# Performance work log

Measured on AMD Instinct MI355X. Metric: run time of the kernel, lower is better.

## Reference

```python
import jax, jax.numpy as jnp
import numpy as np

DIM = 1024
HEADS = 16
HEAD_DIM = DIM // HEADS
SCALE = HEAD_DIM ** -0.5


def setup_inputs() -> dict:
    key = jax.random.key(0)
    ks = jax.random.split(key, 9)
    B, S, D = 2, 2048, DIM
    std = 1.0 / np.sqrt(D)
    Z = jax.random.normal(ks[0], (B, S, D), dtype=jnp.float32)
    Wq = jax.random.uniform(ks[1], (D, D), jnp.float32, -std, std)
    bq = jax.random.uniform(ks[2], (D,), jnp.float32, -std, std)
    Wk = jax.random.uniform(ks[3], (D, D), jnp.float32, -std, std)
    bk = jax.random.uniform(ks[4], (D,), jnp.float32, -std, std)
    Wv = jax.random.uniform(ks[5], (D, D), jnp.float32, -std, std)
    bv = jax.random.uniform(ks[6], (D,), jnp.float32, -std, std)
    Wo = jax.random.uniform(ks[7], (D, D), jnp.float32, -std, std)
    bo = jax.random.uniform(ks[8], (D,), jnp.float32, -std, std)
    return {"Z": Z, "Wq": Wq, "bq": bq, "Wk": Wk, "bk": bk,
            "Wv": Wv, "bv": bv, "Wo": Wo, "bo": bo}


def reference(Z, Wq, bq, Wk, bk, Wv, bv, Wo, bo):
    B, S, D = Z.shape
    H, Hd = HEADS, HEAD_DIM
    # torch Linear: y = x @ W.T + b
    Q = (Z @ Wq.T + bq).reshape(B, S, H, Hd).transpose(0, 2, 1, 3)  # [B,H,S,Hd]
    K = (Z @ Wk.T + bk).reshape(B, S, H, Hd).transpose(0, 2, 1, 3)
    V = (Z @ Wv.T + bv).reshape(B, S, H, Hd).transpose(0, 2, 1, 3)
    scores = jnp.einsum('bhqd,bhkd->bhqk', Q, K) * SCALE  # [B,H,S,S]
    weights = jax.nn.softmax(scores, axis=-1)
    weights = jnp.nan_to_num(weights, nan=0.0)
    # dropout=0.0 -> identity (eval mode)
    out = jnp.einsum('bhqk,bhkd->bhqd', weights, V)  # [B,H,S,Hd]
    out = out.transpose(0, 2, 1, 3).reshape(B, S, D)
    return out @ Wo.T + bo
```

## Files before the change

kernel.cpp:

```cpp
#include <hip/hip_runtime.h>
#include <hip/hip_bf16.h>
#include <stdint.h>

typedef unsigned short u16;
typedef __bf16 bf16x8 __attribute__((ext_vector_type(8)));
typedef float f32x4 __attribute__((ext_vector_type(4)));
typedef float f32x16 __attribute__((ext_vector_type(16)));

#define D_MODEL 1024
#define SEQ     2048
#define NB      2
#define NH      16
#define HD      64
#define M_TOT   (NB*SEQ)
#define QSCALE  (0.125f * 1.44269504088896f)
#define DEFER_THR 8.0f

__device__ __forceinline__ u16 f2bf(float f) {
  union { __bf16 b; u16 u; } cv; cv.b = (__bf16)f; return cv.u;
}
__device__ __forceinline__ float exp2_fast(float x) {
  return __builtin_amdgcn_exp2f(x);
}

__device__ __forceinline__ void async_copy16(void* lds_dst, const void* gsrc) {
  __builtin_amdgcn_global_load_lds(
      (const __attribute__((address_space(1))) unsigned int*)gsrc,
      (__attribute__((address_space(3))) unsigned int*)lds_dst, 16, 0, 0);
}

__global__ void cvt_all(const float* __restrict__ Z,  const float* __restrict__ Wq,
                        const float* __restrict__ Wk, const float* __restrict__ Wv,
                        const float* __restrict__ Wo,
                        u16* __restrict__ Zb,  u16* __restrict__ Wqb,
                        u16* __restrict__ Wkb, u16* __restrict__ Wvb,
                        u16* __restrict__ Wob)
{
  int i = blockIdx.x * 256 + threadIdx.x;
  const float* src; u16* dst; int off;
  if (i < (1 << 20)) { src = Z; dst = Zb; off = i; }
  else {
    int j = i - (1 << 20);
    int seg = j >> 18; off = j & ((1 << 18) - 1);
    src = (seg == 0) ? Wq : (seg == 1) ? Wk : (seg == 2) ? Wv : Wo;
    dst = (seg == 0) ? Wqb : (seg == 1) ? Wkb : (seg == 2) ? Wvb : Wob;
  }
  float4 v = reinterpret_cast<const float4*>(src)[off];
  ushort4 o;
  o.x = f2bf(v.x); o.y = f2bf(v.y); o.z = f2bf(v.z); o.w = f2bf(v.w);
  reinterpret_cast<ushort4*>(dst)[off] = o;
}

template<int F32OUT, int TRANSV>
__global__ __launch_bounds__(256, 3)
void gemm_bt(const u16* __restrict__ A,
             const u16* __restrict__ B0, const u16* __restrict__ B1, const u16* __restrict__ B2,
             const float* __restrict__ bias0, const float* __restrict__ bias1, const float* __restrict__ bias2,
             void* __restrict__ C0, void* __restrict__ C1, void* __restrict__ C2,
             float s0, float s1, float s2,
             int M, int N, int K)
{
  (void)M;
  const int z = blockIdx.z;
  const u16* Bt = (z == 0) ? B0 : ((z == 1) ? B1 : B2);
  const float* bias = (z == 0) ? bias0 : ((z == 1) ? bias1 : bias2);
  void* Cout = (z == 0) ? C0 : ((z == 1) ? C1 : C2);
  const float oscl = (z == 0) ? s0 : ((z == 1) ? s1 : s2);
  const bool vswap = TRANSV && (z == 2);

  __shared__ u16 lds_a[2][128*32];
  __shared__ u16 lds_b[2][128*32];

  const int tid = threadIdx.x;
  const int w = tid >> 6, lane = tid & 63;
  const int l15 = lane & 15, lhi = lane >> 4;
  const int m0 = blockIdx.y * 128, n0 = blockIdx.x * 128;
  const int wm = w >> 1, wn = w & 1;

  f32x4 acc[4][4] = {};

  auto stage = [&](int buf, int kt) {
    const int k0 = kt * 32;
    #pragma unroll
    for (int i = 0; i < 2; ++i) {
      const int base = (w*2 + i) * 1024;
      const int pos  = base + (lane << 4);
      const int row  = pos >> 6;
      const int slot = (pos >> 4) & 3;
      const int ss   = slot ^ ((row >> 1) & 3);
      async_copy16((char*)lds_a[buf] + base,
                   (const char*)(A  + (size_t)(m0 + row) * K + k0 + ss*8));
      async_copy16((char*)lds_b[buf] + base,
                   (const char*)(Bt + (size_t)(n0 + row) * K + k0 + ss*8));
    }
  };

  auto compute = [&](int buf) {
    bf16x8 af[4], bf[4];
    #pragma unroll
    for (int mi = 0; mi < 4; ++mi) {
      const int row = wm*64 + mi*16 + l15;
      const int s   = lhi ^ ((row >> 1) & 3);
      af[mi] = *reinterpret_cast<const bf16x8*>((const char*)lds_a[buf] + row*64 + s*16);
    }
    #pragma unroll
    for (int ni = 0; ni < 4; ++ni) {
      const int row = wn*64 + ni*16 + l15;
      const int s   = lhi ^ ((row >> 1) & 3);
      bf[ni] = *reinterpret_cast<const bf16x8*>((const char*)lds_b[buf] + row*64 + s*16);
    }
    if (vswap) {
      #pragma unroll
      for (int mi = 0; mi < 4; ++mi)
        #pragma unroll
        for (int ni = 0; ni < 4; ++ni)
          acc[mi][ni] = __builtin_amdgcn_mfma_f32_16x16x32_bf16(bf[ni], af[mi], acc[mi][ni], 0, 0, 0);
    } else {
      #pragma unroll
      for (int mi = 0; mi < 4; ++mi)
        #pragma unroll
        for (int ni = 0; ni < 4; ++ni)
          acc[mi][ni] = __builtin_amdgcn_mfma_f32_16x16x32_bf16(af[mi], bf[ni], acc[mi][ni], 0, 0, 0);
    }
  };

  stage(0, 0);
  __syncthreads();
  const int nk = K >> 5;
  for (int kt = 0; kt < nk; ++kt) {
    if (kt + 1 < nk) stage((kt + 1) & 1, kt + 1);
    compute(kt & 1);
    __syncthreads();
  }

  if (vswap) {
    #pragma unroll
    for (int mi = 0; mi < 4; ++mi) {
      const int sglob = m0 + wm*64 + mi*16 + l15;
      const int b2 = sglob >> 11, s = sglob & (SEQ - 1);
      #pragma unroll
      for (int ni = 0; ni < 4; ++ni) {
        #pragma unroll
        for (int r = 0; r < 4; ++r) {
          const int dglob = n0 + wn*64 + ni*16 + (lhi << 2) + r;
          const int hh = dglob >> 6, dd = dglob & 63;
          const float v = acc[mi][ni][r] + bias[dglob];
          reinterpret_cast<u16*>(Cout)[((size_t)(b2*NH + hh)*HD + dd)*SEQ + s] = f2bf(v);
        }
      }
    }
  } else {
    #pragma unroll
    for (int mi = 0; mi < 4; ++mi) {
      const int rowb = m0 + wm*64 + mi*16 + (lhi << 2);
      #pragma unroll
      for (int ni = 0; ni < 4; ++ni) {
        const int col = n0 + wn*64 + ni*16 + l15;
        const float bb = bias[col];
        #pragma unroll
        for (int r = 0; r < 4; ++r) {
          const float v = (acc[mi][ni][r] + bb) * oscl;
          if (F32OUT)
            reinterpret_cast<float*>(Cout)[(size_t)(rowb + r) * N + col] = v;
          else
            reinterpret_cast<u16*>(Cout)[(size_t)(rowb + r) * N + col] = f2bf(v);
        }
      }
    }
  }
}

__global__ __launch_bounds__(256, 2)
void attn32(const u16* __restrict__ Qb, const u16* __restrict__ Kb,
            const u16* __restrict__ Vt, u16* __restrict__ Ob)
{
  __shared__ u16 vt[2][64*64];
  __shared__ u16 kt[2][64*64];

  const int tid = threadIdx.x;
  const int w = tid >> 6, lane = tid & 63;
  const int l31 = lane & 31, hi = lane >> 5;
  const int bh = blockIdx.y, b = bh >> 4, h = bh & 15;
  const int qrow = blockIdx.x * 128 + w * 32 + l31;

  bf16x8 qf[4];
  {
    const u16* qp = Qb + (size_t)(b*SEQ + qrow) * D_MODEL + h*HD + hi*8;
    #pragma unroll
    for (int kc = 0; kc < 4; ++kc)
      qf[kc] = *reinterpret_cast<const bf16x8*>(qp + kc*16);
  }

  const u16* Vtg = Vt + (size_t)bh * HD * SEQ;
  const u16* Kg  = Kb + (size_t)(b*SEQ) * D_MODEL + h*HD;

  float mrun = -1e30f, lrun = 0.f;
  f32x16 o0 = {}, o1 = {};

  auto stageKV = [&](int buf, int kv0) {
    #pragma unroll
    for (int i = 0; i < 2; ++i) {
      const int c = i*256 + tid;
      const int d = c >> 3;
      const int sl = c & 7;
      const int sg = sl ^ (d & 7);
      async_copy16((char*)vt[buf] + (size_t)(i*256 + w*64)*16,
                   (const char*)(Vtg + (size_t)d*SEQ + kv0 + sg*8));
    }
    #pragma unroll
    for (int i = 0; i < 2; ++i) {
      const int c = i*256 + tid;
      const int key = c >> 3;
      const int sl = c & 7;
      const int sg = sl ^ (key & 7);
      async_copy16((char*)kt[buf] + (size_t)(i*256 + w*64)*16,
                   (const char*)(Kg + (size_t)(kv0 + key)*D_MODEL + sg*8));
    }
  };

  stageKV(0, 0);
  __syncthreads();
  int buf = 0;

  for (int kv0 = 0; kv0 < SEQ; kv0 += 64) {
    if (kv0 + 64 < SEQ) stageKV(buf ^ 1, kv0 + 64);

    f32x16 s0 = {}, s1 = {};
    {
      const char* kbp = (const char*)kt[buf];
      #pragma unroll
      for (int kc = 0; kc < 4; ++kc) {
        const int sw = (kc*2 + hi) ^ (l31 & 7);
        bf16x8 ka0 = *reinterpret_cast<const bf16x8*>(kbp + (size_t)(l31*8 + sw)*16);
        s0 = __builtin_amdgcn_mfma_f32_32x32x16_bf16(ka0, qf[kc], s0, 0, 0, 0);
        bf16x8 ka1 = *reinterpret_cast<const bf16x8*>(kbp + (size_t)((l31+32)*8 + sw)*16);
        s1 = __builtin_amdgcn_mfma_f32_32x32x16_bf16(ka1, qf[kc], s1, 0, 0, 0);
      }
    }

    float tmax = s0[0];
    #pragma unroll
    for (int r = 1; r < 16; ++r) tmax = fmaxf(tmax, s0[r]);
    #pragma unroll
    for (int r = 0; r < 16; ++r) tmax = fmaxf(tmax, s1[r]);
    tmax = fmaxf(tmax, __shfl_xor(tmax, 32));
    if (!__all(tmax - mrun <= DEFER_THR)) {
      const float mnew = fmaxf(mrun, tmax);
      const float a = exp2_fast(mrun - mnew);
      lrun *= a;
      #pragma unroll
      for (int r = 0; r < 16; ++r) { o0[r] *= a; o1[r] *= a; }
      mrun = mnew;
    }
    float rs = 0.f;
    #pragma unroll
    for (int r = 0; r < 16; ++r) { s0[r] = exp2_fast(s0[r] - mrun); rs += s0[r]; }
    #pragma unroll
    for (int r = 0; r < 16; ++r) { s1[r] = exp2_fast(s1[r] - mrun); rs += s1[r]; }
    rs += __shfl_xor(rs, 32);
    lrun += rs;

    unsigned pwA[2][8];
    #pragma unroll
    for (int a4 = 0; a4 < 4; ++a4)
      #pragma unroll
      for (int zz = 0; zz < 2; ++zz) {
        pwA[0][a4*2+zz] = (unsigned)f2bf(s0[4*a4+2*zz]) | ((unsigned)f2bf(s0[4*a4+2*zz+1]) << 16);
        pwA[1][a4*2+zz] = (unsigned)f2bf(s1[4*a4+2*zz]) | ((unsigned)f2bf(s1[4*a4+2*zz+1]) << 16);
      }

    const char* vb = (const char*)vt[buf];
    #pragma unroll
    for (int ks = 0; ks < 4; ++ks) {
      const int kb = ks >> 1, sm = ks & 1;
      unsigned keep0 = hi ? pwA[kb][(2*sm+1)*2+0] : pwA[kb][(2*sm)*2+0];
      unsigned keep1 = hi ? pwA[kb][(2*sm+1)*2+1] : pwA[kb][(2*sm)*2+1];
      unsigned send0 = hi ? pwA[kb][(2*sm)*2+0]   : pwA[kb][(2*sm+1)*2+0];
      unsigned send1 = hi ? pwA[kb][(2*sm)*2+1]   : pwA[kb][(2*sm+1)*2+1];
      unsigned recv0 = (unsigned)__shfl_xor((int)send0, 32);
      unsigned recv1 = (unsigned)__shfl_xor((int)send1, 32);
      union { bf16x8 f; unsigned u[4]; } pf;
      pf.u[0] = hi ? recv0 : keep0;
      pf.u[1] = hi ? recv1 : keep1;
      pf.u[2] = hi ? keep0 : recv0;
      pf.u[3] = hi ? keep1 : recv1;

      const int slg = ks*2 + hi;
      const int sw  = slg ^ (l31 & 7);
      bf16x8 va0 = *reinterpret_cast<const bf16x8*>(vb + (size_t)(l31*8 + sw)*16);
      bf16x8 va1 = *reinterpret_cast<const bf16x8*>(vb + (size_t)((l31+32)*8 + sw)*16);

      o0 = __builtin_amdgcn_mfma_f32_32x32x16_bf16(va0, pf.f, o0, 0, 0, 0);
      o1 = __builtin_amdgcn_mfma_f32_32x32x16_bf16(va1, pf.f, o1, 0, 0, 0);
    }

    __syncthreads();
    buf ^= 1;
  }

  const float inv = 1.0f / lrun;
  u16* op = Ob + (size_t)(b*SEQ + qrow) * D_MODEL + h*HD;
  #pragma unroll
  for (int a4 = 0; a4 < 4; ++a4) {
    ushort4 v0, v1;
    v0.x = f2bf(o0[4*a4+0]*inv); v0.y = f2bf(o0[4*a4+1]*inv);
    v0.z = f2bf(o0[4*a4+2]*inv); v0.w = f2bf(o0[4*a4+3]*inv);
    v1.x = f2bf(o1[4*a4+0]*inv); v1.y = f2bf(o1[4*a4+1]*inv);
    v1.z = f2bf(o1[4*a4+2]*inv); v1.w = f2bf(o1[4*a4+3]*inv);
    *reinterpret_cast<ushort4*>(op + 8*a4 + 4*hi)      = v0;
    *reinterpret_cast<ushort4*>(op + 32 + 8*a4 + 4*hi) = v1;
  }
}

extern "C" void kernel_launch(void* const* d_in, const int* in_sizes, int n_in,
                              void* d_out, int out_size, void* d_ws, size_t ws_size,
                              hipStream_t stream)
{
  (void)in_sizes; (void)n_in; (void)out_size;
  const float* Z  = (const float*)d_in[0];
  const float* Wq = (const float*)d_in[1];
  const float* bq = (const float*)d_in[2];
  const float* Wk = (const float*)d_in[3];
  const float* bk = (const float*)d_in[4];
  const float* Wv = (const float*)d_in[5];
  const float* bv = (const float*)d_in[6];
  const float* Wo = (const float*)d_in[7];
  const float* bo = (const float*)d_in[8];
  float* out = (float*)d_out;

  const size_t needed = (size_t)(M_TOT*D_MODEL)*2*5 + (size_t)(D_MODEL*D_MODEL)*2*4;
  if (ws_size < needed) return;

  u16* Zb  = (u16*)d_ws;
  u16* Wqb = Zb  + (size_t)M_TOT*D_MODEL;
  u16* Wkb = Wqb + (size_t)D_MODEL*D_MODEL;
  u16* Wvb = Wkb + (size_t)D_MODEL*D_MODEL;
  u16* Wob = Wvb + (size_t)D_MODEL*D_MODEL;
  u16* Qb  = Wob + (size_t)D_MODEL*D_MODEL;
  u16* Kb  = Qb  + (size_t)M_TOT*D_MODEL;
  u16* Vt  = Kb  + (size_t)M_TOT*D_MODEL;
  u16* Ab  = Vt  + (size_t)M_TOT*D_MODEL;

  cvt_all<<<dim3(8192), 256, 0, stream>>>(Z, Wq, Wk, Wv, Wo, Zb, Wqb, Wkb, Wvb, Wob);

  dim3 gproj(D_MODEL/128, M_TOT/128, 3);
  gemm_bt<0,1><<<gproj, 256, 0, stream>>>(Zb, Wqb, Wkb, Wvb, bq, bk, bv,
                                          (void*)Qb, (void*)Kb, (void*)Vt,
                                          QSCALE, 1.0f, 1.0f,
                                          M_TOT, D_MODEL, D_MODEL);

  dim3 gattn(SEQ/128, NB*NH);
  attn32<<<gattn, 256, 0, stream>>>(Qb, Kb, Vt, Ab);

  dim3 gout(D_MODEL/128, M_TOT/128, 1);
  gemm_bt<1,0><<<gout, 256, 0, stream>>>(Ab, Wob, Wob, Wob, bo, bo, bo,
                                         (void*)out, (void*)out, (void*)out,
                                         1.0f, 1.0f, 1.0f,
                                         M_TOT, D_MODEL, D_MODEL);
}
```

Baseline: 239.0 us.

## Triple-buffer LDS tiles with partial vmcnt waits in GEMM and attention

Both the projection GEMM and the attention kernel move from double to triple buffering of their LDS tiles, prefetching two tiles ahead. The full __syncthreads is replaced by an explicit s_waitcnt vmcnt(N) that waits only for the current tile's async global-to-LDS loads, followed by a raw s_barrier. The aim is to keep more memory traffic in flight and stop stalling on loads that are not yet needed. In exchange, each block uses more LDS, which may limit occupancy. Correctness depends on each stage issuing exactly four loads per thread and on the compiler not reordering or adding memory ops.

```diff
diff --git a/kernel.cpp b/kernel.cpp
--- a/kernel.cpp
+++ b/kernel.cpp
@@ -27,6 +27,15 @@
   __builtin_amdgcn_global_load_lds(
       (const __attribute__((address_space(1))) unsigned int*)gsrc,
       (__attribute__((address_space(3))) unsigned int*)lds_dst, 16, 0, 0);
+}
+
+__device__ __forceinline__ void wait_tile(int kt, int nk) {
+  if (kt + 2 < nk)      { asm volatile("s_waitcnt vmcnt(8)" ::: "memory"); }
+  else if (kt + 1 < nk) { asm volatile("s_waitcnt vmcnt(4)" ::: "memory"); }
+  else                  { asm volatile("s_waitcnt vmcnt(0)" ::: "memory"); }
+  __builtin_amdgcn_sched_barrier(0);
+  __builtin_amdgcn_s_barrier();
+  __builtin_amdgcn_sched_barrier(0);
 }
 
 __global__ void cvt_all(const float* __restrict__ Z,  const float* __restrict__ Wq,
@@ -68,8 +77,8 @@
   const float oscl = (z == 0) ? s0 : ((z == 1) ? s1 : s2);
   const bool vswap = TRANSV && (z == 2);
 
-  __shared__ u16 lds_a[2][128*32];
-  __shared__ u16 lds_b[2][128*32];
+  __shared__ u16 lds_a[3][128*32];
+  __shared__ u16 lds_b[3][128*32];
 
   const int tid = threadIdx.x;
   const int w = tid >> 6, lane = tid & 63;
@@ -124,13 +133,16 @@
     }
   };
 
+  const int nk = K >> 5;
   stage(0, 0);
-  __syncthreads();
-  const int nk = K >> 5;
+  stage(1, 1);
   for (int kt = 0; kt < nk; ++kt) {
-    if (kt + 1 < nk) stage((kt + 1) & 1, kt + 1);
-    compute(kt & 1);
-    __syncthreads();
+    const int cb = kt % 3;
+    if (kt + 2 < nk) stage((kt + 2) % 3, kt + 2);
+    wait_tile(kt, nk);
+    compute(cb);
+    __builtin_amdgcn_sched_barrier(0);
+    __builtin_amdgcn_s_barrier();
   }
 
   if (vswap) {
@@ -174,8 +186,8 @@
 void attn32(const u16* __restrict__ Qb, const u16* __restrict__ Kb,
             const u16* __restrict__ Vt, u16* __restrict__ Ob)
 {
-  __shared__ u16 vt[2][64*64];
-  __shared__ u16 kt[2][64*64];
+  __shared__ u16 vt[3][64*64];
+  __shared__ u16 kt[3][64*64];
 
   const int tid = threadIdx.x;
   const int w = tid >> 6, lane = tid & 63;
@@ -218,16 +230,18 @@
     }
   };
 
+  const int nt = SEQ / 64;
   stageKV(0, 0);
-  __syncthreads();
-  int buf = 0;
-
-  for (int kv0 = 0; kv0 < SEQ; kv0 += 64) {
-    if (kv0 + 64 < SEQ) stageKV(buf ^ 1, kv0 + 64);
+  stageKV(1, 64);
+
+  for (int t = 0; t < nt; ++t) {
+    const int cb = t % 3;
+    if (t + 2 < nt) stageKV((t + 2) % 3, (t + 2) * 64);
+    wait_tile(t, nt);
 
     f32x16 s0 = {}, s1 = {};
     {
-      const char* kbp = (const char*)kt[buf];
+      const char* kbp = (const char*)kt[cb];
       #pragma unroll
       for (int kc = 0; kc < 4; ++kc) {
         const int sw = (kc*2 + hi) ^ (l31 & 7);
@@ -269,7 +283,7 @@
         pwA[1][a4*2+zz] = (unsigned)f2bf(s1[4*a4+2*zz]) | ((unsigned)f2bf(s1[4*a4+2*zz+1]) << 16);
       }
 
-    const char* vb = (const char*)vt[buf];
+    const char* vb = (const char*)vt[cb];
     #pragma unroll
     for (int ks = 0; ks < 4; ++ks) {
       const int kb = ks >> 1, sm = ks & 1;
@@ -294,8 +308,8 @@
       o1 = __builtin_amdgcn_mfma_f32_32x32x16_bf16(va1, pf.f, o1, 0, 0, 0);
     }
 
-    __syncthreads();
-    buf ^= 1;
+    __builtin_amdgcn_sched_barrier(0);
+    __builtin_amdgcn_s_barrier();
   }
 
   const float inv = 1.0f / lrun;
```

Result: no change. 237.2 us (-0.7%).
